# Optimization experiments

Measured on AMD Instinct MI355X. Metric: run time of the kernel, lower is better.

Reference implementation:

```python
import jax, jax.numpy as jnp
import numpy as np

HEADS = 8
DIM_HEAD = 64
NUM_MEM_KV = 4

def rmsnorm(x, g):
    # F.normalize(x, dim=1) * g * sqrt(C): L2-normalize over channel dim with eps clamp
    n = jnp.sqrt(jnp.sum(x * x, axis=1, keepdims=True))
    return x / jnp.maximum(n, 1e-12) * g * (x.shape[1] ** 0.5)

def setup_inputs() -> dict:
    key = jax.random.key(0)
    ks = jax.random.split(key, 7)
    b, c, h, w = 32, 512, 32, 32
    hidden = HEADS * DIM_HEAD
    x = jax.random.normal(ks[0], (b, c, h, w), jnp.float32)
    g_in = 1.0 + 0.02 * jax.random.normal(ks[1], (1, c, 1, 1), jnp.float32)
    w_qkv = jax.random.normal(ks[2], (3 * hidden, c), jnp.float32) * (c ** -0.5)
    mem_kv = jax.random.normal(ks[3], (2, HEADS, DIM_HEAD, NUM_MEM_KV), jnp.float32)
    w_out = jax.random.normal(ks[4], (c, hidden), jnp.float32) * (hidden ** -0.5)
    b_out = 0.01 * jax.random.normal(ks[5], (c,), jnp.float32)
    g_out = 1.0 + 0.02 * jax.random.normal(ks[6], (1, c, 1, 1), jnp.float32)
    return {"x": x, "g_in": g_in, "w_qkv": w_qkv, "mem_kv": mem_kv,
            "w_out": w_out, "b_out": b_out, "g_out": g_out}

def reference(x, g_in, w_qkv, mem_kv, w_out, b_out, g_out):
    b, c, h, w = x.shape
    scale = DIM_HEAD ** -0.5
    xn = rmsnorm(x, g_in)
    # 1x1 conv (no bias) == channel GEMM
    qkv = jnp.einsum('bchw,oc->bohw', xn, w_qkv)
    q, k, v = jnp.split(qkv, 3, axis=1)
    to_heads = lambda t: t.reshape(b, HEADS, DIM_HEAD, h * w)  # b (h c) x y -> b h c (xy)
    q, k, v = map(to_heads, (q, k, v))
    mk = jnp.broadcast_to(mem_kv[0], (b,) + mem_kv[0].shape)
    mv = jnp.broadcast_to(mem_kv[1], (b,) + mem_kv[1].shape)
    k = jnp.concatenate([mk, k], axis=-1)
    v = jnp.concatenate([mv, v], axis=-1)
    q = jax.nn.softmax(q, axis=-2) * scale   # softmax over feature dim d
    k = jax.nn.softmax(k, axis=-1)           # softmax over sequence dim n
    context = jnp.einsum('bhdn,bhen->bhde', k, v)
    out = jnp.einsum('bhde,bhdn->bhen', context, q)
    out = out.reshape(b, HEADS * DIM_HEAD, h, w)
    out = jnp.einsum('bchw,oc->bohw', out, w_out) + b_out[None, :, None, None]
    return rmsnorm(out, g_out)
```

## Files before the change

kernel.cpp:

```cpp
#include <hip/hip_runtime.h>
#include <hip/hip_bf16.h>


#define AS1 __attribute__((address_space(1)))
#define AS3 __attribute__((address_space(3)))

using short8 = __attribute__((ext_vector_type(8))) short;
using usht4  = __attribute__((ext_vector_type(4))) unsigned short;
using f32x4  = __attribute__((ext_vector_type(4))) float;

__device__ __forceinline__ unsigned short f2bf(float f) {
  unsigned int u = __float_as_uint(f);
  u += 0x7fffu + ((u >> 16) & 1u);
  return (unsigned short)(u >> 16);
}
__device__ __forceinline__ float bf2f(unsigned short s) {
  return __uint_as_float(((unsigned int)s) << 16);
}

__global__ __launch_bounds__(256, 4)
void norm_r(const float* __restrict__ X, float* __restrict__ R) {
  __shared__ float part[32][33];
  const int t = threadIdx.x;
  const int b = blockIdx.x >> 5;
  const int pos0 = (blockIdx.x & 31) * 32;
  const int pg = t & 7, cg = t >> 3;
  const float* xp = X + ((size_t)b * 512 + (size_t)cg * 16) * 1024 + pos0 + pg * 4;
  f32x4 s = {0.f, 0.f, 0.f, 0.f};
#pragma unroll
  for (int i = 0; i < 16; ++i) {
    f32x4 v = *(const f32x4*)(xp + (size_t)i * 1024);
    s += v * v;
  }
  part[cg][pg * 4 + 0] = s.x;
  part[cg][pg * 4 + 1] = s.y;
  part[cg][pg * 4 + 2] = s.z;
  part[cg][pg * 4 + 3] = s.w;
  __syncthreads();
  if (t < 32) {
    float tot = 0.f;
#pragma unroll
    for (int j = 0; j < 32; ++j) tot += part[j][t];
    R[(size_t)b * 1024 + pos0 + t] = 22.627416998f / fmaxf(sqrtf(tot), 1e-12f);
  }
}

__global__ __launch_bounds__(256, 4)
void norm_r_bf16(const unsigned short* __restrict__ X, float* __restrict__ R) {
  __shared__ float part[16][64];
  const int t = threadIdx.x;
  const int b = blockIdx.x >> 4;
  const int pos0 = (blockIdx.x & 15) * 64;
  const int pg = t & 15, cg = t >> 4;
  const unsigned short* xp =
      X + ((size_t)b * 512 + (size_t)cg * 32) * 1024 + pos0 + pg * 4;
  float s0 = 0.f, s1 = 0.f, s2 = 0.f, s3 = 0.f;
#pragma unroll 8
  for (int i = 0; i < 32; ++i) {
    usht4 v = *(const usht4*)(xp + (size_t)i * 1024);
    float a = bf2f(v.x), bb = bf2f(v.y), c = bf2f(v.z), d = bf2f(v.w);
    s0 += a * a; s1 += bb * bb; s2 += c * c; s3 += d * d;
  }
  part[cg][pg * 4 + 0] = s0;
  part[cg][pg * 4 + 1] = s1;
  part[cg][pg * 4 + 2] = s2;
  part[cg][pg * 4 + 3] = s3;
  __syncthreads();
  if (t < 64) {
    float tot = 0.f;
#pragma unroll
    for (int j = 0; j < 16; ++j) tot += part[j][t];
    R[(size_t)b * 1024 + pos0 + t] = 22.627416998f / fmaxf(sqrtf(tot), 1e-12f);
  }
}

__global__ __launch_bounds__(256, 4)
void xn_transpose(const float* __restrict__ X, const float* __restrict__ R,
                  unsigned short* __restrict__ XT) {
  __shared__ float tile[64][65];
  const int t = threadIdx.x;
  const int b = blockIdx.z, cb = blockIdx.y, pb = blockIdx.x;
  {
    const int p = t & 63, cg = t >> 6;
    const float r = R[(size_t)b * 1024 + pb * 64 + p];
    const float* xp = X + ((size_t)b * 512 + (size_t)(cb * 64 + cg * 16)) * 1024 + pb * 64 + p;
#pragma unroll
    for (int i = 0; i < 16; ++i)
      tile[cg * 16 + i][p] = xp[(size_t)i * 1024] * r;
  }
  __syncthreads();
#pragma unroll
  for (int k = 0; k < 2; ++k) {
    const int idx = k * 256 + t;
    const int p = idx >> 3, c8 = idx & 7;
    short8 v;
#pragma unroll
    for (int j = 0; j < 8; ++j) v[j] = (short)f2bf(tile[c8 * 8 + j][p]);
    *(short8*)(XT + ((size_t)b * 1024 + pb * 64 + p) * 512 + cb * 64 + c8 * 8) = v;
  }
}

__global__ __launch_bounds__(256, 4)
void cast_wqkv(const float* __restrict__ W, const float* __restrict__ g,
               unsigned short* __restrict__ O) {
  int i = blockIdx.x * 256 + threadIdx.x;
  O[i] = f2bf(W[i] * g[i & 511]);
}
__global__ __launch_bounds__(256, 4)
void cast_w(const float* __restrict__ W, unsigned short* __restrict__ O, int n) {
  int i = blockIdx.x * 256 + threadIdx.x;
  if (i < n) O[i] = f2bf(W[i]);
}

template <int MTOT, bool SPLIT3, bool BIAS>
__global__ __launch_bounds__(512, 2)
void gemm_bt(const unsigned short* __restrict__ A,
             const unsigned short* __restrict__ Ball,
             unsigned short* __restrict__ O0, unsigned short* __restrict__ O1,
             unsigned short* __restrict__ O2, const float* __restrict__ bias) {
  __shared__ __align__(16) unsigned short smem[65536];
  const int t = threadIdx.x;
  const int lane = t & 63, w = t >> 6;
  const int wm = w >> 2, wn = w & 3;
  const int mt = blockIdx.x >> 2, nt = blockIdx.x & 3;
  const int b = blockIdx.y;
  const unsigned short* Ag = A + (size_t)(mt * 256) * 512;
  const unsigned short* Bg = Ball + ((size_t)b * 1024 + (size_t)nt * 256) * 512;

  const int srow = w * 16 + (lane >> 2);
  const int schunk8 = ((lane & 3) ^ ((lane >> 3) & 3)) * 8;
  const int fr = lane & 15;
  const int slotoff = (((lane >> 4) ^ ((lane >> 1) & 3)) << 3);
  const int aBase = (wm * 128 + fr) * 32 + slotoff;
  const int bBase = (wn * 64 + fr) * 32 + slotoff;

  f32x4 acc[8][4] = {};

  auto STAGE = [&](int kt, int kh, int isB) {
    const unsigned short* Xg = isB ? Bg : Ag;
    unsigned short* plane = smem + (kt & 1) * 32768 + isB * 16384 + kh * 8192;
    const size_t kofs = (size_t)((kt & 7) * 64 + kh * 32 + schunk8);
#pragma unroll
    for (int j = 0; j < 2; ++j)
      __builtin_amdgcn_global_load_lds(
          (const AS1 unsigned int*)(Xg + (size_t)(j * 128 + srow) * 512 + kofs),
          (AS3 unsigned int*)(plane + (j * 128 + w * 16) * 32), 16, 0, 0);
  };

#define GBAR() asm volatile("" ::: "memory"); \
               __builtin_amdgcn_s_barrier();  \
               asm volatile("" ::: "memory")
#define MFMA_BF16 __builtin_amdgcn_mfma_f32_16x16x32_bf16

  STAGE(0, 0, 0); STAGE(0, 0, 1); STAGE(0, 1, 0); STAGE(0, 1, 1);
  asm volatile("s_waitcnt vmcnt(4)" ::: "memory");
  GBAR();

#pragma unroll 1
  for (int kt = 0; kt < 8; ++kt) {
    const unsigned short* lAp = smem + (kt & 1) * 32768;
    const unsigned short* lBp = lAp + 16384;
    const int ktn = kt + 1;
    short8 af[8], bf0, bf1;

#pragma unroll
    for (int i = 0; i < 8; ++i)
      af[i] = *(const short8*)(lAp + aBase + i * 512);
    bf0 = *(const short8*)(lBp + bBase);
    bf1 = *(const short8*)(lBp + bBase + 512);
    STAGE(ktn, 0, 0);
    GBAR();
    __builtin_amdgcn_sched_barrier(0);
    __builtin_amdgcn_s_setprio(1);
#pragma unroll
    for (int i = 0; i < 8; ++i) {
      acc[i][0] = MFMA_BF16(af[i], bf0, acc[i][0], 0, 0, 0);
      acc[i][1] = MFMA_BF16(af[i], bf1, acc[i][1], 0, 0, 0);
    }
    __builtin_amdgcn_s_setprio(0);
    GBAR();

    bf0 = *(const short8*)(lBp + bBase + 1024);
    bf1 = *(const short8*)(lBp + bBase + 1536);
    STAGE(ktn, 0, 1);
    asm volatile("s_waitcnt vmcnt(4)" ::: "memory");
    GBAR();
    __builtin_amdgcn_sched_barrier(0);
    __builtin_amdgcn_s_setprio(1);
#pragma unroll
    for (int i = 0; i < 8; ++i) {
      acc[i][2] = MFMA_BF16(af[i], bf0, acc[i][2], 0, 0, 0);
      acc[i][3] = MFMA_BF16(af[i], bf1, acc[i][3], 0, 0, 0);
    }
    __builtin_amdgcn_s_setprio(0);
    GBAR();

#pragma unroll
    for (int i = 0; i < 8; ++i)
      af[i] = *(const short8*)(lAp + 8192 + aBase + i * 512);
    bf0 = *(const short8*)(lBp + 8192 + bBase);
    bf1 = *(const short8*)(lBp + 8192 + bBase + 512);
    STAGE(ktn, 1, 0);
    GBAR();
    __builtin_amdgcn_sched_barrier(0);
    __builtin_amdgcn_s_setprio(1);
#pragma unroll
    for (int i = 0; i < 8; ++i) {
      acc[i][0] = MFMA_BF16(af[i], bf0, acc[i][0], 0, 0, 0);
      acc[i][1] = MFMA_BF16(af[i], bf1, acc[i][1], 0, 0, 0);
    }
    __builtin_amdgcn_s_setprio(0);
    GBAR();

    bf0 = *(const short8*)(lBp + 8192 + bBase + 1024);
    bf1 = *(const short8*)(lBp + 8192 + bBase + 1536);
    STAGE(ktn, 1, 1);
    asm volatile("s_waitcnt vmcnt(4)" ::: "memory");
    GBAR();
    __builtin_amdgcn_sched_barrier(0);
    __builtin_amdgcn_s_setprio(1);
#pragma unroll
    for (int i = 0; i < 8; ++i) {
      acc[i][2] = MFMA_BF16(af[i], bf0, acc[i][2], 0, 0, 0);
      acc[i][3] = MFMA_BF16(af[i], bf1, acc[i][3], 0, 0, 0);
    }
    __builtin_amdgcn_s_setprio(0);
    GBAR();
  }

  asm volatile("s_waitcnt vmcnt(0)" ::: "memory");
  __syncthreads();
  unsigned short* Cw = smem + w * 8192;
  const int g = lane >> 4, l15 = lane & 15;
#pragma unroll
  for (int i = 0; i < 8; ++i)
#pragma unroll
    for (int j = 0; j < 4; ++j) {
      const int cs = ((j ^ g) << 4) + l15;
#pragma unroll
      for (int r = 0; r < 4; ++r) {
        const int row = i * 16 + g * 4 + r;
        float v = acc[i][j][r];
        if (BIAS) v += bias[mt * 256 + wm * 128 + row];
        Cw[row * 64 + cs] = f2bf(v);
      }
    }
  unsigned short* OgW;
  if (SPLIT3) {
    const int sec = mt >> 1;
    unsigned short* base = (sec == 0) ? O0 : ((sec == 1) ? O1 : O2);
    OgW = base + ((size_t)b * 512 + (size_t)((mt & 1) * 256 + wm * 128)) * 1024 +
          nt * 256 + wn * 64;
  } else {
    OgW = O0 + ((size_t)b * MTOT + (size_t)(mt * 256 + wm * 128)) * 1024 +
          nt * 256 + wn * 64;
  }
#pragma unroll
  for (int p = 0; p < 16; ++p) {
    const int row = p * 8 + (lane >> 3);
    const int q2 = (row >> 2) & 3;
    const int slot = (lane & 7) ^ (q2 << 1);
    short8 v = *(const short8*)(Cw + row * 64 + slot * 8);
    *(short8*)(OgW + (size_t)row * 1024 + (lane & 7) * 8) = v;
  }
#undef GBAR
#undef MFMA_BF16
}

__global__ __launch_bounds__(256, 2)
void attn_kernel(const unsigned short* __restrict__ Qp,
                 const unsigned short* __restrict__ Kp,
                 const unsigned short* __restrict__ Vp,
                 const float* __restrict__ memkv,
                 unsigned short* __restrict__ outT) {
  __shared__ char smem[36608];
  unsigned short* bufA = (unsigned short*)smem;
  unsigned short* bufB = (unsigned short*)(smem + 9216);
  float* Pl   = (float*)(smem + 18432);
  float* Pc   = (float*)(smem + 18432);
  float* csS  = (float*)(smem + 21504);
  float* msum = (float*)(smem + 35072);
  float* rsI  = (float*)(smem + 36096);
  const int t = threadIdx.x;
  const int lane = t & 63, wave = t >> 6;
  const int b = blockIdx.x >> 3, h = blockIdx.x & 7;
  const size_t hb = ((size_t)b * 512 + (size_t)h * 64) * 1024;
  const unsigned short* Qg = Qp + hb;
  const unsigned short* Kg = Kp + hb;
  const unsigned short* Vg = Vp + hb;
  const float* mk = memkv + (size_t)h * 256;
  const float* mv = memkv + 2048 + (size_t)h * 256;

  float rsum[2] = {0.f, 0.f};
  f32x4 cacc[4] = {};

  for (int it = 0; it < 17; ++it) {
    if (it == 0) {
      const int d = t & 63, j = t >> 6;
      const float ev = __expf(mk[d * 4 + j]);
      msum[d * 4 + j] = ev;
      bufA[d * 72 + j] = f2bf(ev);
      bufB[d * 72 + j] = f2bf(mv[d * 4 + j]);
      for (int c2 = 4 + j; c2 < 64; c2 += 4) {
        bufA[d * 72 + c2] = 0;
        bufB[d * 72 + c2] = 0;
      }
    } else {
      const int c0 = (it - 1) * 64;
#pragma unroll
      for (int z = 0; z < 2; ++z) {
        const int d = z * 32 + (t >> 3), ch = t & 7;
        short8 kv = *(const short8*)(Kg + (size_t)d * 1024 + c0 + ch * 8);
        short8 pk;
        float ssum = 0.f;
#pragma unroll
        for (int j = 0; j < 8; ++j) {
          const float e = __expf(bf2f((unsigned short)kv[j]));
          ssum += e;
          pk[j] = (short)f2bf(e);
        }
        rsum[z] += ssum;
        *(short8*)(bufA + d * 72 + ch * 8) = pk;
        short8 vv = *(const short8*)(Vg + (size_t)d * 1024 + c0 + ch * 8);
        *(short8*)(bufB + d * 72 + ch * 8) = vv;
      }
    }
    __syncthreads();
#pragma unroll
    for (int ks = 0; ks < 2; ++ks) {
      short8 a = *(const short8*)(bufA + (wave * 16 + (lane & 15)) * 72 +
                                  ks * 32 + (lane >> 4) * 8);
#pragma unroll
      for (int et = 0; et < 4; ++et) {
        short8 bb = *(const short8*)(bufB + (et * 16 + (lane & 15)) * 72 +
                                     ks * 32 + (lane >> 4) * 8);
        cacc[et] = __builtin_amdgcn_mfma_f32_16x16x32_bf16(a, bb, cacc[et], 0, 0, 0);
      }
    }
    __syncthreads();
  }

  Pl[t]       = rsum[0];
  Pl[256 + t] = rsum[1];
  __syncthreads();
  if (t < 64) {
    float s = 0.f;
#pragma unroll
    for (int ch = 0; ch < 8; ++ch) s += Pl[t * 8 + ch];
    s += msum[t * 4] + msum[t * 4 + 1] + msum[t * 4 + 2] + msum[t * 4 + 3];
    rsI[t] = 1.0f / s;
  }
  __syncthreads();

  unsigned short* CT = bufB;
#pragma unroll
  for (int et = 0; et < 4; ++et)
#pragma unroll
    for (int r = 0; r < 4; ++r) {
      const int d = wave * 16 + (lane >> 4) * 4 + r;
      const int e = et * 16 + (lane & 15);
      CT[e * 72 + d] = f2bf(cacc[et][r] * rsI[d]);
    }
  __syncthreads();

  short8 a0 = *(const short8*)(CT + (wave * 16 + (lane & 15)) * 72 + (lane >> 4) * 8);
  short8 a1 = *(const short8*)(CT + (wave * 16 + (lane & 15)) * 72 + 32 + (lane >> 4) * 8);
  unsigned short* oBase = outT + (size_t)b * 1024 * 512 + h * 64;

  for (int pt = 0; pt < 16; ++pt) {
    {
      const int p = lane, dq = wave;
      float cp = 0.f;
#pragma unroll
      for (int i2 = 0; i2 < 8; ++i2) {
        const int d0 = dq * 16 + i2 * 2;
        const float e0 = __expf(bf2f(Qg[(size_t)d0 * 1024 + pt * 64 + p]));
        const float e1 = __expf(bf2f(Qg[(size_t)(d0 + 1) * 1024 + pt * 64 + p]));
        cp += e0 + e1;
        const unsigned int pk =
            (unsigned int)f2bf(e0) | ((unsigned int)f2bf(e1) << 16);
        *(unsigned int*)(bufA + p * 72 + d0) = pk;
      }
      Pc[dq * 64 + p] = cp;
    }
    __syncthreads();
    if (t < 64) csS[t] = 0.125f / (Pc[t] + Pc[64 + t] + Pc[128 + t] + Pc[192 + t]);
    __syncthreads();
#pragma unroll
    for (int ps = 0; ps < 4; ++ps) {
      f32x4 oc = {};
      short8 b0 = *(const short8*)(bufA + (ps * 16 + (lane & 15)) * 72 + (lane >> 4) * 8);
      short8 b1 = *(const short8*)(bufA + (ps * 16 + (lane & 15)) * 72 + 32 + (lane >> 4) * 8);
      oc = __builtin_amdgcn_mfma_f32_16x16x32_bf16(a0, b0, oc, 0, 0, 0);
      oc = __builtin_amdgcn_mfma_f32_16x16x32_bf16(a1, b1, oc, 0, 0, 0);
      const float cs = csS[ps * 16 + (lane & 15)];
      const unsigned long long pk =
          (unsigned long long)f2bf(oc[0] * cs) |
          ((unsigned long long)f2bf(oc[1] * cs) << 16) |
          ((unsigned long long)f2bf(oc[2] * cs) << 32) |
          ((unsigned long long)f2bf(oc[3] * cs) << 48);
      const int p = pt * 64 + ps * 16 + (lane & 15);
      *(unsigned long long*)(oBase + (size_t)p * 512 + wave * 16 + (lane >> 4) * 4) = pk;
    }
    __syncthreads();
  }
}

__global__ __launch_bounds__(256, 4)
void final_scale_bf16(const unsigned short* __restrict__ P,
                      const float* __restrict__ R, const float* __restrict__ G,
                      float* __restrict__ O) {
  const size_t f = ((size_t)blockIdx.x * 256 + threadIdx.x) * 4;
  const int p = (int)(f & 1023);
  const int c = (int)((f >> 10) & 511);
  const int b = (int)(f >> 19);
  usht4 v = *(const usht4*)(P + f);
  const f32x4 r = *(const f32x4*)(R + (size_t)b * 1024 + p);
  const float g = G[c];
  f32x4 o;
  o.x = bf2f(v.x) * r.x * g;
  o.y = bf2f(v.y) * r.y * g;
  o.z = bf2f(v.z) * r.z * g;
  o.w = bf2f(v.w) * r.w * g;
  *(f32x4*)(O + f) = o;
}

extern "C" void kernel_launch(void* const* d_in, const int* in_sizes, int n_in,
                              void* d_out, int out_size, void* d_ws, size_t ws_size,
                              hipStream_t stream) {
  (void)in_sizes; (void)n_in; (void)out_size; (void)ws_size;
  const float* x     = (const float*)d_in[0];
  const float* g_in  = (const float*)d_in[1];
  const float* w_qkv = (const float*)d_in[2];
  const float* memkv = (const float*)d_in[3];
  const float* w_out = (const float*)d_in[4];
  const float* b_out = (const float*)d_in[5];
  const float* g_out = (const float*)d_in[6];
  float* out = (float*)d_out;

  char* ws = (char*)d_ws;
  float* r1           = (float*)ws;
  float* r2           = (float*)(ws + 131072);
  unsigned short* wqb = (unsigned short*)(ws + 262144);
  unsigned short* wob = (unsigned short*)(ws + 1835008);
  unsigned short* xnT = (unsigned short*)(ws + 2359296);
  unsigned short* Qp  = (unsigned short*)(ws + 35913728);
  unsigned short* outT = xnT;
  unsigned short* pre  = Qp;
  unsigned short* Kp  = (unsigned short*)d_out;
  unsigned short* Vp  = (unsigned short*)d_out + 16777216;

  norm_r<<<1024, 256, 0, stream>>>(x, r1);
  xn_transpose<<<dim3(16, 8, 32), 256, 0, stream>>>(x, r1, xnT);
  cast_wqkv<<<3072, 256, 0, stream>>>(w_qkv, g_in, wqb);
  cast_w<<<1024, 256, 0, stream>>>(w_out, wob, 262144);
  gemm_bt<1536, true, false><<<dim3(24, 32), 512, 0, stream>>>(
      wqb, xnT, Qp, Kp, Vp, nullptr);
  attn_kernel<<<256, 256, 0, stream>>>(Qp, Kp, Vp, memkv, outT);
  gemm_bt<512, false, true><<<dim3(8, 32), 512, 0, stream>>>(
      wob, outT, pre, nullptr, nullptr, b_out);
  norm_r_bf16<<<512, 256, 0, stream>>>(pre, r2);
  final_scale_bf16<<<16384, 256, 0, stream>>>(pre, r2, g_out, out);
}
```

Baseline: 282.6 us.

## Restage GEMM tiles as full 64-wide K rows with XOR swizzle and two-phase prefetch

Changes the LDS tile layout from two 32-element K halves per row to one 64-element K row per tile row, with an 8-way XOR swizzle on 16-byte chunks. Each wave's global loads now cover whole 128-byte row segments. Prefetch of the next K-tile is regrouped into two phases (rows 0-127, then 128-255), with one full vmcnt(0) wait at the end of each iteration instead of partial waits. This aims for more contiguous global accesses and fewer bank conflicts on fragment reads, but it delays synchronisation to the end of each iteration and may expose load latency.

After: 282.6 us. Within noise of the previous version (+0.0%).

```diff
diff --git a/kernel.cpp b/kernel.cpp
--- a/kernel.cpp
+++ b/kernel.cpp
@@ -127,24 +127,29 @@
   const unsigned short* Ag = A + (size_t)(mt * 256) * 512;
   const unsigned short* Bg = Ball + ((size_t)b * 1024 + (size_t)nt * 256) * 512;
 
-  const int srow = w * 16 + (lane >> 2);
-  const int schunk8 = ((lane & 3) ^ ((lane >> 3) & 3)) * 8;
+  const int srow = w * 8 + (lane >> 3);
+  const int schunk = ((lane & 7) ^ (lane >> 3)) * 8;
+  const unsigned short* Asrc = Ag + (size_t)srow * 512 + schunk;
+  const unsigned short* Bsrc = Bg + (size_t)srow * 512 + schunk;
+
   const int fr = lane & 15;
-  const int slotoff = (((lane >> 4) ^ ((lane >> 1) & 3)) << 3);
-  const int aBase = (wm * 128 + fr) * 32 + slotoff;
-  const int bBase = (wn * 64 + fr) * 32 + slotoff;
+  const int sw0 = ((lane >> 4) ^ (fr & 7)) << 3;
+  const int sw1 = sw0 ^ 32;
+  const int aRow = (wm * 128 + fr) * 64;
+  const int bRow = (wn * 64 + fr) * 64;
 
   f32x4 acc[8][4] = {};
 
-  auto STAGE = [&](int kt, int kh, int isB) {
-    const unsigned short* Xg = isB ? Bg : Ag;
-    unsigned short* plane = smem + (kt & 1) * 32768 + isB * 16384 + kh * 8192;
-    const size_t kofs = (size_t)((kt & 7) * 64 + kh * 32 + schunk8);
+  auto STAGE = [&](int kt, int half, int isB) {
+    const unsigned short* Xs = isB ? Bsrc : Asrc;
+    unsigned short* dst = smem + (kt & 1) * 32768 + isB * 16384 +
+                          half * 8192 + w * 512;
+    const size_t ko = (size_t)kt * 64 + (size_t)(half * 128) * 512;
 #pragma unroll
     for (int j = 0; j < 2; ++j)
       __builtin_amdgcn_global_load_lds(
-          (const AS1 unsigned int*)(Xg + (size_t)(j * 128 + srow) * 512 + kofs),
-          (AS3 unsigned int*)(plane + (j * 128 + w * 16) * 32), 16, 0, 0);
+          (const AS1 unsigned int*)(Xs + ko + (size_t)(j * 64) * 512),
+          (AS3 unsigned int*)(dst + j * 4096), 16, 0, 0);
   };
 
 #define GBAR() asm volatile("" ::: "memory"); \
@@ -153,22 +158,21 @@
 #define MFMA_BF16 __builtin_amdgcn_mfma_f32_16x16x32_bf16
 
   STAGE(0, 0, 0); STAGE(0, 0, 1); STAGE(0, 1, 0); STAGE(0, 1, 1);
-  asm volatile("s_waitcnt vmcnt(4)" ::: "memory");
+  asm volatile("s_waitcnt vmcnt(0)" ::: "memory");
   GBAR();
 
 #pragma unroll 1
   for (int kt = 0; kt < 8; ++kt) {
     const unsigned short* lAp = smem + (kt & 1) * 32768;
     const unsigned short* lBp = lAp + 16384;
-    const int ktn = kt + 1;
     short8 af[8], bf0, bf1;
 
 #pragma unroll
     for (int i = 0; i < 8; ++i)
-      af[i] = *(const short8*)(lAp + aBase + i * 512);
-    bf0 = *(const short8*)(lBp + bBase);
-    bf1 = *(const short8*)(lBp + bBase + 512);
-    STAGE(ktn, 0, 0);
+      af[i] = *(const short8*)(lAp + aRow + i * 1024 + sw0);
+    bf0 = *(const short8*)(lBp + bRow + sw0);
+    bf1 = *(const short8*)(lBp + bRow + 1024 + sw0);
+    if (kt < 7) { STAGE(kt + 1, 0, 0); STAGE(kt + 1, 0, 1); }
     GBAR();
     __builtin_amdgcn_sched_barrier(0);
     __builtin_amdgcn_s_setprio(1);
@@ -180,10 +184,9 @@
     __builtin_amdgcn_s_setprio(0);
     GBAR();
 
-    bf0 = *(const short8*)(lBp + bBase + 1024);
-    bf1 = *(const short8*)(lBp + bBase + 1536);
-    STAGE(ktn, 0, 1);
-    asm volatile("s_waitcnt vmcnt(4)" ::: "memory");
+    bf0 = *(const short8*)(lBp + bRow + 2048 + sw0);
+    bf1 = *(const short8*)(lBp + bRow + 3072 + sw0);
+    if (kt < 7) { STAGE(kt + 1, 1, 0); STAGE(kt + 1, 1, 1); }
     GBAR();
     __builtin_amdgcn_sched_barrier(0);
     __builtin_amdgcn_s_setprio(1);
@@ -197,10 +200,9 @@
 
 #pragma unroll
     for (int i = 0; i < 8; ++i)
-      af[i] = *(const short8*)(lAp + 8192 + aBase + i * 512);
-    bf0 = *(const short8*)(lBp + 8192 + bBase);
-    bf1 = *(const short8*)(lBp + 8192 + bBase + 512);
-    STAGE(ktn, 1, 0);
+      af[i] = *(const short8*)(lAp + aRow + i * 1024 + sw1);
+    bf0 = *(const short8*)(lBp + bRow + sw1);
+    bf1 = *(const short8*)(lBp + bRow + 1024 + sw1);
     GBAR();
     __builtin_amdgcn_sched_barrier(0);
     __builtin_amdgcn_s_setprio(1);
@@ -212,10 +214,9 @@
     __builtin_amdgcn_s_setprio(0);
     GBAR();
 
-    bf0 = *(const short8*)(lBp + 8192 + bBase + 1024);
-    bf1 = *(const short8*)(lBp + 8192 + bBase + 1536);
-    STAGE(ktn, 1, 1);
-    asm volatile("s_waitcnt vmcnt(4)" ::: "memory");
+    bf0 = *(const short8*)(lBp + bRow + 2048 + sw1);
+    bf1 = *(const short8*)(lBp + bRow + 3072 + sw1);
+    asm volatile("s_waitcnt vmcnt(0)" ::: "memory");
     GBAR();
     __builtin_amdgcn_sched_barrier(0);
     __builtin_amdgcn_s_setprio(1);
@@ -228,7 +229,6 @@
     GBAR();
   }
 
-  asm volatile("s_waitcnt vmcnt(0)" ::: "memory");
   __syncthreads();
   unsigned short* Cw = smem + w * 8192;
   const int g = lane >> 4, l15 = lane & 15;
```
